# Performance work log

Measured on AMD Instinct MI355X. Metric: run time of the kernel, lower is better.

Reference implementation:

```python
import jax, jax.numpy as jnp
import numpy as np

B, N, D = 64, 1024, 1024

def setup_inputs() -> dict:
    key = jax.random.key(0)
    k1, k2, k3, k4, k5 = jax.random.split(key, 5)
    s = 1.0 / np.sqrt(D)
    return {
        "h_t": jax.random.normal(k1, (B, D), dtype=jnp.float32),
        "keys": jax.random.normal(k2, (B, N, D), dtype=jnp.float32),
        "W_h": jax.random.uniform(k3, (D, D), jnp.float32, -s, s),
        "W_k": jax.random.uniform(k4, (D, D), jnp.float32, -s, s),
        "v": jax.random.uniform(k5, (D,), jnp.float32, -s, s),
    }

def reference(h_t, keys, W_h, W_k, v):
    # W_h(h_t): [B, D]; W_k(keys): [B, N, D]  (nn.Linear computes x @ W.T)
    qh = h_t @ W_h.T                       # [B, D]
    kh = jnp.einsum('bnd,ed->bne', keys, W_k)  # [B, N, D]
    energy = jnp.tanh(qh[:, None, :] + kh)     # [B, N, D]
    scores = jnp.einsum('bnd,d->bn', energy, v)  # [B, N]
    alpha = jax.nn.softmax(scores, axis=-1)      # [B, N]
    context = jnp.einsum('bn,bnd->bd', alpha, keys)  # [B, D]
    return (context, alpha)
```

## Files before the change

kernel.cpp:

```cpp
#include <hip/hip_runtime.h>
#include <math.h>

#define BB 64
#define NN 1024
#define DD 1024

typedef __bf16 bf16x8 __attribute__((ext_vector_type(8)));
typedef _Float16 f16x8 __attribute__((ext_vector_type(8)));
typedef float f32x4 __attribute__((ext_vector_type(4)));
typedef unsigned short u16x8 __attribute__((ext_vector_type(8)));

#define GLOAD_LDS16(g, l)                                                  \
    __builtin_amdgcn_global_load_lds(                                      \
        (const __attribute__((address_space(1))) unsigned int*)(g),        \
        (__attribute__((address_space(3))) unsigned int*)(l), 16, 0, 0)

__device__ __forceinline__ float fast_tanh(float x) {
    return 1.f - 2.f / (__expf(2.f * x) + 1.f);
}


__global__ __launch_bounds__(256) void k_wk(const float* __restrict__ W_k,
                                            _Float16* __restrict__ wkT) {
    const int et = blockIdx.x;
    const int ks = blockIdx.y;
    const int t = threadIdx.x;
    const float* src = W_k + (size_t)et * 128 * DD;
    _Float16* dst = wkT + (size_t)et * 32 * 4096;
    const int p0 = t * 8;
    const int n0 = p0 >> 5;
    const int k0 = p0 & 31;
    const int ksw = (k0 >> 3) ^ ((n0 >> 1) & 3);
    for (int kt = ks * 8; kt < ks * 8 + 8; ++kt) {
#pragma unroll
        for (int r = 0; r < 2; ++r) {
            const int n = n0 + r * 64;
            const float4* s4 = (const float4*)(src + (size_t)n * DD + kt * 32 + k0);
            float4 a = s4[0], b4 = s4[1];
            f16x8 h = {(_Float16)a.x,  (_Float16)a.y,  (_Float16)a.z,  (_Float16)a.w,
                       (_Float16)b4.x, (_Float16)b4.y, (_Float16)b4.z, (_Float16)b4.w};
            *(f16x8*)(dst + (size_t)kt * 4096 + n * 32 + ksw * 8) = h;
        }
    }
}

__global__ __launch_bounds__(256) void k_qh(const float* __restrict__ h_t,
                                            const float* __restrict__ W_h,
                                            float* __restrict__ qh,
                                            float* __restrict__ scores) {
    __shared__ float hs[DD];
    __shared__ float red2[128];
    const int b = blockIdx.x;
    const int et = blockIdx.y;
    const int t = threadIdx.x;
    if (t < 128) scores[b * NN + et * 128 + t] = 0.f;
    ((float4*)hs)[t] = ((const float4*)(h_t + (size_t)b * DD))[t];
    __syncthreads();
    const int el = t & 127;
    const int half = t >> 7;
    const int e = et * 128 + el;
    const float4* wrow = (const float4*)(W_h + (size_t)e * DD) + half * 128;
    const float* hp = hs + half * 512;
    float acc = 0.f;
#pragma unroll 4
    for (int k4 = 0; k4 < 128; ++k4) {
        float4 wv = wrow[k4];
        acc = fmaf(wv.x, hp[4 * k4 + 0], acc);
        acc = fmaf(wv.y, hp[4 * k4 + 1], acc);
        acc = fmaf(wv.z, hp[4 * k4 + 2], acc);
        acc = fmaf(wv.w, hp[4 * k4 + 3], acc);
    }
    if (half == 1) red2[el] = acc;
    __syncthreads();
    if (half == 0) qh[(size_t)b * DD + e] = acc + red2[el];
}

#define SPAD2 40
__global__ __launch_bounds__(256, 3) void k_scf(const float* __restrict__ keys,
                                                const _Float16* __restrict__ wkT,
                                                const float* __restrict__ v,
                                                const float* __restrict__ qh,
                                                float* __restrict__ scores) {
    __shared__ _Float16 As[128 * SPAD2];
    __shared__ _Float16 Bs[2 * 4096];
    __shared__ float vs[128];
    __shared__ float qs[128];
    __shared__ float red[128][2];

    const int tid = threadIdx.x;
    const int cp = blockIdx.x >> 3;
    const int nt = blockIdx.x & 7;
    const int b = blockIdx.y;
    const int e0 = cp * 128;

    if (tid < 128) {
        vs[tid] = v[e0 + tid];
        qs[tid] = qh[b * DD + e0 + tid];
    }

    const float* Ag = keys + ((size_t)b * NN + nt * 128) * DD;
    const char* Bg = (const char*)(wkT + (size_t)cp * 32 * 4096) + tid * 16;
    char* BsB = (char*)Bs;

    const int w = tid >> 6, lane = tid & 63;
    const int wm = w & 1, we = w >> 1;
    const int lcol = lane & 15, quad = lane >> 4;
    const int qx8 = (quad ^ ((lcol >> 1) & 3)) * 8;
    const int srow = tid >> 1, sseg = tid & 1;
    const float* Ap = Ag + (size_t)srow * DD + sseg * 16;

    f32x4 acc[4][4];
#pragma unroll
    for (int mi = 0; mi < 4; ++mi)
#pragma unroll
        for (int ni = 0; ni < 4; ++ni) acc[mi][ni] = (f32x4){0.f, 0.f, 0.f, 0.f};

    float4 pa[4];
#pragma unroll
    for (int i = 0; i < 4; ++i) pa[i] = ((const float4*)Ap)[i];
    GLOAD_LDS16(Bg, BsB + tid * 16);
    GLOAD_LDS16(Bg + 4096, BsB + 4096 + tid * 16);

#pragma unroll 1
    for (int kt = 0; kt < 32; ++kt) {
        const int slot = kt & 1;
        __builtin_amdgcn_s_barrier();
        __builtin_amdgcn_sched_barrier(0);
        f16x8 h0 = {(_Float16)pa[0].x, (_Float16)pa[0].y, (_Float16)pa[0].z, (_Float16)pa[0].w,
                    (_Float16)pa[1].x, (_Float16)pa[1].y, (_Float16)pa[1].z, (_Float16)pa[1].w};
        f16x8 h1 = {(_Float16)pa[2].x, (_Float16)pa[2].y, (_Float16)pa[2].z, (_Float16)pa[2].w,
                    (_Float16)pa[3].x, (_Float16)pa[3].y, (_Float16)pa[3].z, (_Float16)pa[3].w};
        *(f16x8*)&As[srow * SPAD2 + sseg * 16] = h0;
        *(f16x8*)&As[srow * SPAD2 + sseg * 16 + 8] = h1;
        if (kt + 1 < 32) {
            const float* Apn = Ap + (kt + 1) * 32;
#pragma unroll
            for (int i = 0; i < 4; ++i) pa[i] = ((const float4*)Apn)[i];
            GLOAD_LDS16(Bg + (size_t)(kt + 1) * 8192, BsB + (slot ^ 1) * 8192 + tid * 16);
            GLOAD_LDS16(Bg + (size_t)(kt + 1) * 8192 + 4096,
                        BsB + (slot ^ 1) * 8192 + 4096 + tid * 16);
            asm volatile("s_waitcnt vmcnt(6) lgkmcnt(0)" ::: "memory");
        } else {
            asm volatile("s_waitcnt vmcnt(0) lgkmcnt(0)" ::: "memory");
        }
        __builtin_amdgcn_s_barrier();
        __builtin_amdgcn_sched_barrier(0);

        f16x8 af[4], bf[4];
#pragma unroll
        for (int mi = 0; mi < 4; ++mi)
            af[mi] = *(const f16x8*)&As[(wm * 64 + mi * 16 + lcol) * SPAD2 + quad * 8];
#pragma unroll
        for (int ni = 0; ni < 4; ++ni)
            bf[ni] = *(const f16x8*)&Bs[slot * 4096 + (we * 64 + ni * 16 + lcol) * 32 + qx8];
        asm volatile("s_waitcnt lgkmcnt(0)" ::: "memory");
        __builtin_amdgcn_sched_barrier(0);
        __builtin_amdgcn_s_setprio(1);
#pragma unroll
        for (int mi = 0; mi < 4; ++mi)
#pragma unroll
            for (int ni = 0; ni < 4; ++ni)
                acc[mi][ni] = __builtin_amdgcn_mfma_f32_16x16x32_f16(af[mi], bf[ni], acc[mi][ni], 0, 0, 0);
        __builtin_amdgcn_s_setprio(0);
        __builtin_amdgcn_sched_barrier(0);
    }

    float part[4][4];
#pragma unroll
    for (int mi = 0; mi < 4; ++mi)
#pragma unroll
        for (int r = 0; r < 4; ++r) part[mi][r] = 0.f;
#pragma unroll
    for (int mi = 0; mi < 4; ++mi)
#pragma unroll
        for (int ni = 0; ni < 4; ++ni) {
            const int e = we * 64 + ni * 16 + lcol;
            const float vv = vs[e];
            const float qv = qs[e];
#pragma unroll
            for (int r = 0; r < 4; ++r)
                part[mi][r] += vv * fast_tanh(qv + acc[mi][ni][r]);
        }
#pragma unroll
    for (int mi = 0; mi < 4; ++mi)
#pragma unroll
        for (int r = 0; r < 4; ++r) {
            float p = part[mi][r];
            p += __shfl_xor(p, 1);
            p += __shfl_xor(p, 2);
            p += __shfl_xor(p, 4);
            p += __shfl_xor(p, 8);
            if (lcol == 0) red[wm * 64 + mi * 16 + quad * 4 + r][we] = p;
        }
    __syncthreads();
    if (tid < 128) atomicAdd(&scores[b * NN + nt * 128 + tid], red[tid][0] + red[tid][1]);
}

__global__ __launch_bounds__(256) void k_sm(const float* __restrict__ scores,
                                            float* __restrict__ alpha) {
    const int b = blockIdx.x;
    const int t = threadIdx.x;
    float x[4];
    float m = -1e30f;
#pragma unroll
    for (int j = 0; j < 4; ++j) {
        x[j] = scores[b * NN + t + 256 * j];
        m = fmaxf(m, x[j]);
    }
#pragma unroll
    for (int mask = 32; mask >= 1; mask >>= 1) m = fmaxf(m, __shfl_xor(m, mask));
    __shared__ float wred[4];
    __shared__ float wsum[4];
    const int wv = t >> 6;
    if ((t & 63) == 0) wred[wv] = m;
    __syncthreads();
    m = fmaxf(fmaxf(wred[0], wred[1]), fmaxf(wred[2], wred[3]));
    float s = 0.f;
#pragma unroll
    for (int j = 0; j < 4; ++j) {
        x[j] = expf(x[j] - m);
        s += x[j];
    }
#pragma unroll
    for (int mask = 32; mask >= 1; mask >>= 1) s += __shfl_xor(s, mask);
    if ((t & 63) == 0) wsum[wv] = s;
    __syncthreads();
    s = wsum[0] + wsum[1] + wsum[2] + wsum[3];
    const float inv = 1.f / s;
#pragma unroll
    for (int j = 0; j < 4; ++j) alpha[b * NN + t + 256 * j] = x[j] * inv;
}

__global__ __launch_bounds__(256) void k_ctx(const float* __restrict__ keys,
                                             const float* __restrict__ alpha,
                                             float* __restrict__ context) {
    __shared__ float al[NN];
    __shared__ float red[16][72];
    const int dc = blockIdx.x;
    const int b = blockIdx.y;
    const int t = threadIdx.x;
#pragma unroll
    for (int j = 0; j < 4; ++j) al[t + 256 * j] = alpha[b * NN + t + 256 * j];
    __syncthreads();

    const int ng = t >> 4;
    const int dq = t & 15;
    const float* kp = keys + (size_t)b * NN * DD + dc * 64 + dq * 4;
    float4 acc = {0.f, 0.f, 0.f, 0.f};
#pragma unroll 4
    for (int i = 0; i < 64; ++i) {
        const int n = i * 16 + ng;
        float4 kv = *(const float4*)(kp + (size_t)n * DD);
        const float a = al[n];
        acc.x = fmaf(a, kv.x, acc.x);
        acc.y = fmaf(a, kv.y, acc.y);
        acc.z = fmaf(a, kv.z, acc.z);
        acc.w = fmaf(a, kv.w, acc.w);
    }
    *(float4*)&red[ng][dq * 4] = acc;
    __syncthreads();
    if (t < 64) {
        float s = 0.f;
#pragma unroll
        for (int g = 0; g < 16; ++g) s += red[g][t];
        context[(size_t)b * DD + dc * 64 + t] = s;
    }
}

__global__ __launch_bounds__(256) void qh_fb(const float* __restrict__ h_t,
                                             const float* __restrict__ W_h,
                                             float* __restrict__ qh,
                                             float* __restrict__ scores) {
    __shared__ float hs[DD];
    const int b = blockIdx.y;
    const int e = blockIdx.x * 256 + threadIdx.x;
    scores[(blockIdx.y * 4 + blockIdx.x) * 256 + threadIdx.x] = 0.f;
    for (int i = threadIdx.x; i < DD; i += 256) hs[i] = h_t[b * DD + i];
    __syncthreads();
    const float4* wrow = (const float4*)(W_h + (size_t)e * DD);
    float acc = 0.f;
#pragma unroll 4
    for (int k4 = 0; k4 < DD / 4; ++k4) {
        float4 w = wrow[k4];
        acc = fmaf(w.x, hs[4 * k4 + 0], acc);
        acc = fmaf(w.y, hs[4 * k4 + 1], acc);
        acc = fmaf(w.z, hs[4 * k4 + 2], acc);
        acc = fmaf(w.w, hs[4 * k4 + 3], acc);
    }
    qh[b * DD + e] = acc;
}

#define SPAD 40
__device__ __forceinline__ void split16(const float4* __restrict__ src,
                                        unsigned short* hi, unsigned short* lo) {
    float x[16];
    float4 v0 = src[0], v1 = src[1], v2 = src[2], v3 = src[3];
    x[0] = v0.x; x[1] = v0.y; x[2] = v0.z; x[3] = v0.w;
    x[4] = v1.x; x[5] = v1.y; x[6] = v1.z; x[7] = v1.w;
    x[8] = v2.x; x[9] = v2.y; x[10] = v2.z; x[11] = v2.w;
    x[12] = v3.x; x[13] = v3.y; x[14] = v3.z; x[15] = v3.w;
#pragma unroll
    for (int i = 0; i < 16; ++i) {
        unsigned int u = __float_as_uint(x[i]);
        hi[i] = (unsigned short)(u >> 16);
        float hif = __uint_as_float(u & 0xFFFF0000u);
        float lof = x[i] - hif;
        lo[i] = (unsigned short)(__float_as_uint(lof) >> 16);
    }
}

__global__ __launch_bounds__(256, 2) void scores_fb(const float* __restrict__ keys,
                                                    const float* __restrict__ W_k,
                                                    const float* __restrict__ v,
                                                    const float* __restrict__ qh,
                                                    float* __restrict__ scores) {
    __shared__ unsigned short Ah[128 * SPAD];
    __shared__ unsigned short Al[128 * SPAD];
    __shared__ unsigned short Bh[128 * SPAD];
    __shared__ unsigned short Bl[128 * SPAD];
    __shared__ float vs[128];
    __shared__ float qs[128];
    __shared__ float red[128][2];

    const int tid = threadIdx.x;
    const int cp = blockIdx.x;
    const int rt = blockIdx.y;
    const int b = rt >> 3;
    const int n0 = (rt & 7) * 128;
    const int e0 = cp * 128;
    if (tid < 128) {
        vs[tid] = v[e0 + tid];
        qs[tid] = qh[b * DD + e0 + tid];
    }
    const float* Ag = keys + ((size_t)b * NN + n0) * DD;
    const float* Bg = W_k + (size_t)e0 * DD;
    const int w = tid >> 6;
    const int lane = tid & 63;
    const int wm = w & 1;
    const int we = w >> 1;
    const int lcol = lane & 15;
    const int quad = lane >> 4;
    f32x4 acc[4][4];
#pragma unroll
    for (int mi = 0; mi < 4; ++mi)
#pragma unroll
        for (int ni = 0; ni < 4; ++ni) acc[mi][ni] = (f32x4){0.f, 0.f, 0.f, 0.f};
    const int srow = tid >> 1;
    const int sseg = tid & 1;
    float4 pa[4], pb[4];
    {
        const float4* as = (const float4*)(Ag + (size_t)srow * DD + sseg * 16);
        const float4* bs = (const float4*)(Bg + (size_t)srow * DD + sseg * 16);
#pragma unroll
        for (int i = 0; i < 4; ++i) { pa[i] = as[i]; pb[i] = bs[i]; }
    }
    for (int kt = 0; kt < DD / 32; ++kt) {
        __syncthreads();
        {
            unsigned short hi[16], lo[16];
            split16(pa, hi, lo);
            u16x8* dh = (u16x8*)&Ah[srow * SPAD + sseg * 16];
            u16x8* dl = (u16x8*)&Al[srow * SPAD + sseg * 16];
            dh[0] = *(u16x8*)&hi[0]; dh[1] = *(u16x8*)&hi[8];
            dl[0] = *(u16x8*)&lo[0]; dl[1] = *(u16x8*)&lo[8];
            split16(pb, hi, lo);
            u16x8* eh = (u16x8*)&Bh[srow * SPAD + sseg * 16];
            u16x8* el = (u16x8*)&Bl[srow * SPAD + sseg * 16];
            eh[0] = *(u16x8*)&hi[0]; eh[1] = *(u16x8*)&hi[8];
            el[0] = *(u16x8*)&lo[0]; el[1] = *(u16x8*)&lo[8];
        }
        if (kt + 1 < DD / 32) {
            const int k0 = (kt + 1) * 32;
            const float4* as = (const float4*)(Ag + (size_t)srow * DD + k0 + sseg * 16);
            const float4* bs = (const float4*)(Bg + (size_t)srow * DD + k0 + sseg * 16);
#pragma unroll
            for (int i = 0; i < 4; ++i) { pa[i] = as[i]; pb[i] = bs[i]; }
        }
        __syncthreads();
        bf16x8 ah[4], al2[4], bh[4], bl2[4];
#pragma unroll
        for (int mi = 0; mi < 4; ++mi) {
            const int r = wm * 64 + mi * 16 + lcol;
            ah[mi] = *(const bf16x8*)&Ah[r * SPAD + quad * 8];
            al2[mi] = *(const bf16x8*)&Al[r * SPAD + quad * 8];
        }
#pragma unroll
        for (int ni = 0; ni < 4; ++ni) {
            const int r = we * 64 + ni * 16 + lcol;
            bh[ni] = *(const bf16x8*)&Bh[r * SPAD + quad * 8];
            bl2[ni] = *(const bf16x8*)&Bl[r * SPAD + quad * 8];
        }
#pragma unroll
        for (int mi = 0; mi < 4; ++mi)
#pragma unroll
            for (int ni = 0; ni < 4; ++ni) {
                acc[mi][ni] = __builtin_amdgcn_mfma_f32_16x16x32_bf16(ah[mi], bh[ni], acc[mi][ni], 0, 0, 0);
                acc[mi][ni] = __builtin_amdgcn_mfma_f32_16x16x32_bf16(ah[mi], bl2[ni], acc[mi][ni], 0, 0, 0);
                acc[mi][ni] = __builtin_amdgcn_mfma_f32_16x16x32_bf16(al2[mi], bh[ni], acc[mi][ni], 0, 0, 0);
            }
    }
    float part[4][4];
#pragma unroll
    for (int mi = 0; mi < 4; ++mi)
#pragma unroll
        for (int r = 0; r < 4; ++r) part[mi][r] = 0.f;
#pragma unroll
    for (int mi = 0; mi < 4; ++mi)
#pragma unroll
        for (int ni = 0; ni < 4; ++ni) {
            const int e = we * 64 + ni * 16 + lcol;
            const float vv = vs[e];
            const float qv = qs[e];
#pragma unroll
            for (int r = 0; r < 4; ++r)
                part[mi][r] += vv * fast_tanh(qv + acc[mi][ni][r]);
        }
#pragma unroll
    for (int mi = 0; mi < 4; ++mi)
#pragma unroll
        for (int r = 0; r < 4; ++r) {
            float p = part[mi][r];
            p += __shfl_xor(p, 1);
            p += __shfl_xor(p, 2);
            p += __shfl_xor(p, 4);
            p += __shfl_xor(p, 8);
            if (lcol == 0) red[wm * 64 + mi * 16 + quad * 4 + r][we] = p;
        }
    __syncthreads();
    if (tid < 128) atomicAdd(&scores[b * NN + n0 + tid], red[tid][0] + red[tid][1]);
}

__global__ __launch_bounds__(256) void sm_fb(const float* __restrict__ scores,
                                             float* __restrict__ alpha,
                                             float* __restrict__ context) {
    const int b = blockIdx.x;
    const int t = threadIdx.x;
#pragma unroll
    for (int j = 0; j < 4; ++j) context[b * DD + t + 256 * j] = 0.f;
    float x[4];
    float m = -1e30f;
#pragma unroll
    for (int j = 0; j < 4; ++j) {
        x[j] = scores[b * NN + t + 256 * j];
        m = fmaxf(m, x[j]);
    }
#pragma unroll
    for (int mask = 32; mask >= 1; mask >>= 1) m = fmaxf(m, __shfl_xor(m, mask));
    __shared__ float wred[4];
    __shared__ float wsum[4];
    const int wv = t >> 6;
    if ((t & 63) == 0) wred[wv] = m;
    __syncthreads();
    m = fmaxf(fmaxf(wred[0], wred[1]), fmaxf(wred[2], wred[3]));
    float s = 0.f;
#pragma unroll
    for (int j = 0; j < 4; ++j) {
        x[j] = expf(x[j] - m);
        s += x[j];
    }
#pragma unroll
    for (int mask = 32; mask >= 1; mask >>= 1) s += __shfl_xor(s, mask);
    if ((t & 63) == 0) wsum[wv] = s;
    __syncthreads();
    s = wsum[0] + wsum[1] + wsum[2] + wsum[3];
    const float inv = 1.f / s;
#pragma unroll
    for (int j = 0; j < 4; ++j) alpha[b * NN + t + 256 * j] = x[j] * inv;
}

__global__ __launch_bounds__(256) void ctx_fb(const float* __restrict__ keys,
                                              const float* __restrict__ alpha,
                                              float* __restrict__ context) {
    const int b = blockIdx.y;
    const int nc = blockIdx.x;
    const int t = threadIdx.x;
    __shared__ float al[64];
    if (t < 64) al[t] = alpha[b * NN + nc * 64 + t];
    __syncthreads();
    const float4* kp = (const float4*)(keys + ((size_t)b * NN + nc * 64) * DD);
    float4 acc = {0.f, 0.f, 0.f, 0.f};
#pragma unroll 4
    for (int n = 0; n < 64; ++n) {
        const float a = al[n];
        float4 kv = kp[(size_t)n * (DD / 4) + t];
        acc.x = fmaf(a, kv.x, acc.x);
        acc.y = fmaf(a, kv.y, acc.y);
        acc.z = fmaf(a, kv.z, acc.z);
        acc.w = fmaf(a, kv.w, acc.w);
    }
    float* cp = context + b * DD + 4 * t;
    atomicAdd(cp + 0, acc.x);
    atomicAdd(cp + 1, acc.y);
    atomicAdd(cp + 2, acc.z);
    atomicAdd(cp + 3, acc.w);
}

extern "C" void kernel_launch(void* const* d_in, const int* in_sizes, int n_in,
                              void* d_out, int out_size, void* d_ws, size_t ws_size,
                              hipStream_t stream) {
    const float* h_t = (const float*)d_in[0];
    const float* keys = (const float*)d_in[1];
    const float* W_h = (const float*)d_in[2];
    const float* W_k = (const float*)d_in[3];
    const float* v = (const float*)d_in[4];

    float* context = (float*)d_out;
    float* alpha = (float*)d_out + BB * DD;
    float* qh = (float*)d_ws;
    float* scores = (float*)d_ws + BB * DD;

    const size_t wkT_off = (size_t)2 * BB * DD * sizeof(float);
    const size_t need = wkT_off + (size_t)DD * DD * 2;

    if (ws_size >= need) {
        _Float16* wkT = (_Float16*)((char*)d_ws + wkT_off);
        k_wk<<<dim3(8, 4), 256, 0, stream>>>(W_k, wkT);
        k_qh<<<dim3(64, 8), 256, 0, stream>>>(h_t, W_h, qh, scores);
        k_scf<<<dim3(64, 64), 256, 0, stream>>>(keys, wkT, v, qh, scores);
        k_sm<<<BB, 256, 0, stream>>>(scores, alpha);
        k_ctx<<<dim3(16, 64), 256, 0, stream>>>(keys, alpha, context);
    } else {
        qh_fb<<<dim3(4, BB), 256, 0, stream>>>(h_t, W_h, qh, scores);
        scores_fb<<<dim3(8, 512), 256, 0, stream>>>(keys, W_k, v, qh, scores);
        sm_fb<<<BB, 256, 0, stream>>>(scores, alpha, context);
        ctx_fb<<<dim3(16, BB), 256, 0, stream>>>(keys, alpha, context);
    }
}
```

Before: 605.8 us.

## Double K-step per iteration in score GEMM and fuse softmax into context kernel

```diff
diff --git a/kernel.cpp b/kernel.cpp
--- a/kernel.cpp
+++ b/kernel.cpp
@@ -75,14 +75,13 @@
     if (half == 0) qh[(size_t)b * DD + e] = acc + red2[el];
 }
 
-#define SPAD2 40
 __global__ __launch_bounds__(256, 3) void k_scf(const float* __restrict__ keys,
                                                 const _Float16* __restrict__ wkT,
                                                 const float* __restrict__ v,
                                                 const float* __restrict__ qh,
                                                 float* __restrict__ scores) {
-    __shared__ _Float16 As[128 * SPAD2];
-    __shared__ _Float16 Bs[2 * 4096];
+    __shared__ _Float16 As[2 * 4096];
+    __shared__ _Float16 Bs[2 * 8192];
     __shared__ float vs[128];
     __shared__ float qs[128];
     __shared__ float red[128][2];
@@ -107,7 +106,9 @@
     const int lcol = lane & 15, quad = lane >> 4;
     const int qx8 = (quad ^ ((lcol >> 1) & 3)) * 8;
     const int srow = tid >> 1, sseg = tid & 1;
-    const float* Ap = Ag + (size_t)srow * DD + sseg * 16;
+    const float* Ap = Ag + (size_t)srow * DD + sseg * 32;
+    const int awofs = sseg * 4096 + srow * 32;
+    const int aswz = (srow >> 1) & 3;
 
     f32x4 acc[4][4];
 #pragma unroll
@@ -115,54 +116,70 @@
 #pragma unroll
         for (int ni = 0; ni < 4; ++ni) acc[mi][ni] = (f32x4){0.f, 0.f, 0.f, 0.f};
 
-    float4 pa[4];
-#pragma unroll
-    for (int i = 0; i < 4; ++i) pa[i] = ((const float4*)Ap)[i];
-    GLOAD_LDS16(Bg, BsB + tid * 16);
-    GLOAD_LDS16(Bg + 4096, BsB + 4096 + tid * 16);
+    asm volatile("s_waitcnt vmcnt(0) lgkmcnt(0)" ::: "memory");
+    __builtin_amdgcn_sched_barrier(0);
+
+    float4 pa[8];
+#pragma unroll
+    for (int i = 0; i < 8; ++i) pa[i] = ((const float4*)Ap)[i];
+#pragma unroll
+    for (int r = 0; r < 4; ++r) GLOAD_LDS16(Bg + r * 4096, BsB + r * 4096 + tid * 16);
 
 #pragma unroll 1
-    for (int kt = 0; kt < 32; ++kt) {
+    for (int kt = 0; kt < 16; ++kt) {
         const int slot = kt & 1;
         __builtin_amdgcn_s_barrier();
         __builtin_amdgcn_sched_barrier(0);
-        f16x8 h0 = {(_Float16)pa[0].x, (_Float16)pa[0].y, (_Float16)pa[0].z, (_Float16)pa[0].w,
-                    (_Float16)pa[1].x, (_Float16)pa[1].y, (_Float16)pa[1].z, (_Float16)pa[1].w};
-        f16x8 h1 = {(_Float16)pa[2].x, (_Float16)pa[2].y, (_Float16)pa[2].z, (_Float16)pa[2].w,
-                    (_Float16)pa[3].x, (_Float16)pa[3].y, (_Float16)pa[3].z, (_Float16)pa[3].w};
-        *(f16x8*)&As[srow * SPAD2 + sseg * 16] = h0;
-        *(f16x8*)&As[srow * SPAD2 + sseg * 16 + 8] = h1;
-        if (kt + 1 < 32) {
-            const float* Apn = Ap + (kt + 1) * 32;
-#pragma unroll
-            for (int i = 0; i < 4; ++i) pa[i] = ((const float4*)Apn)[i];
-            GLOAD_LDS16(Bg + (size_t)(kt + 1) * 8192, BsB + (slot ^ 1) * 8192 + tid * 16);
-            GLOAD_LDS16(Bg + (size_t)(kt + 1) * 8192 + 4096,
-                        BsB + (slot ^ 1) * 8192 + 4096 + tid * 16);
-            asm volatile("s_waitcnt vmcnt(6) lgkmcnt(0)" ::: "memory");
+        {
+            f16x8 h0 = {(_Float16)pa[0].x, (_Float16)pa[0].y, (_Float16)pa[0].z, (_Float16)pa[0].w,
+                        (_Float16)pa[1].x, (_Float16)pa[1].y, (_Float16)pa[1].z, (_Float16)pa[1].w};
+            f16x8 h1 = {(_Float16)pa[2].x, (_Float16)pa[2].y, (_Float16)pa[2].z, (_Float16)pa[2].w,
+                        (_Float16)pa[3].x, (_Float16)pa[3].y, (_Float16)pa[3].z, (_Float16)pa[3].w};
+            f16x8 h2 = {(_Float16)pa[4].x, (_Float16)pa[4].y, (_Float16)pa[4].z, (_Float16)pa[4].w,
+                        (_Float16)pa[5].x, (_Float16)pa[5].y, (_Float16)pa[5].z, (_Float16)pa[5].w};
+            f16x8 h3 = {(_Float16)pa[6].x, (_Float16)pa[6].y, (_Float16)pa[6].z, (_Float16)pa[6].w,
+                        (_Float16)pa[7].x, (_Float16)pa[7].y, (_Float16)pa[7].z, (_Float16)pa[7].w};
+            *(f16x8*)&As[awofs + ((0 ^ aswz) * 8)] = h0;
+            *(f16x8*)&As[awofs + ((1 ^ aswz) * 8)] = h1;
+            *(f16x8*)&As[awofs + ((2 ^ aswz) * 8)] = h2;
+            *(f16x8*)&As[awofs + ((3 ^ aswz) * 8)] = h3;
+        }
+        if (kt + 1 < 16) {
+            const float* Apn = Ap + (size_t)(kt + 1) * 64;
+#pragma unroll
+            for (int i = 0; i < 8; ++i) pa[i] = ((const float4*)Apn)[i];
+#pragma unroll
+            for (int r = 0; r < 4; ++r)
+                GLOAD_LDS16(Bg + (size_t)(kt + 1) * 16384 + r * 4096,
+                            BsB + (slot ^ 1) * 16384 + r * 4096 + tid * 16);
+            asm volatile("s_waitcnt vmcnt(12) lgkmcnt(0)" ::: "memory");
         } else {
             asm volatile("s_waitcnt vmcnt(0) lgkmcnt(0)" ::: "memory");
         }
         __builtin_amdgcn_s_barrier();
         __builtin_amdgcn_sched_barrier(0);
 
-        f16x8 af[4], bf[4];
-#pragma unroll
-        for (int mi = 0; mi < 4; ++mi)
-            af[mi] = *(const f16x8*)&As[(wm * 64 + mi * 16 + lcol) * SPAD2 + quad * 8];
-#pragma unroll
-        for (int ni = 0; ni < 4; ++ni)
-            bf[ni] = *(const f16x8*)&Bs[slot * 4096 + (we * 64 + ni * 16 + lcol) * 32 + qx8];
-        asm volatile("s_waitcnt lgkmcnt(0)" ::: "memory");
-        __builtin_amdgcn_sched_barrier(0);
-        __builtin_amdgcn_s_setprio(1);
-#pragma unroll
-        for (int mi = 0; mi < 4; ++mi)
+#pragma unroll
+        for (int kh = 0; kh < 2; ++kh) {
+            f16x8 af[4], bf[4];
+#pragma unroll
+            for (int mi = 0; mi < 4; ++mi)
+                af[mi] = *(const f16x8*)&As[kh * 4096 + (wm * 64 + mi * 16 + lcol) * 32 + qx8];
 #pragma unroll
             for (int ni = 0; ni < 4; ++ni)
-                acc[mi][ni] = __builtin_amdgcn_mfma_f32_16x16x32_f16(af[mi], bf[ni], acc[mi][ni], 0, 0, 0);
-        __builtin_amdgcn_s_setprio(0);
-        __builtin_amdgcn_sched_barrier(0);
+                bf[ni] = *(const f16x8*)&Bs[slot * 8192 + kh * 4096 +
+                                            (we * 64 + ni * 16 + lcol) * 32 + qx8];
+            asm volatile("s_waitcnt lgkmcnt(0)" ::: "memory");
+            __builtin_amdgcn_sched_barrier(0);
+            __builtin_amdgcn_s_setprio(1);
+#pragma unroll
+            for (int mi = 0; mi < 4; ++mi)
+#pragma unroll
+                for (int ni = 0; ni < 4; ++ni)
+                    acc[mi][ni] = __builtin_amdgcn_mfma_f32_16x16x32_f16(af[mi], bf[ni], acc[mi][ni], 0, 0, 0);
+            __builtin_amdgcn_s_setprio(0);
+            __builtin_amdgcn_sched_barrier(0);
+        }
     }
 
     float part[4][4];
@@ -196,10 +213,18 @@
     if (tid < 128) atomicAdd(&scores[b * NN + nt * 128 + tid], red[tid][0] + red[tid][1]);
 }
 
-__global__ __launch_bounds__(256) void k_sm(const float* __restrict__ scores,
-                                            float* __restrict__ alpha) {
-    const int b = blockIdx.x;
+__global__ __launch_bounds__(256) void k_smctx(const float* __restrict__ scores,
+                                               const float* __restrict__ keys,
+                                               float* __restrict__ alpha,
+                                               float* __restrict__ context) {
+    __shared__ float al[NN];
+    __shared__ float red[16][72];
+    __shared__ float wred[4];
+    __shared__ float wsum[4];
+    const int dc = blockIdx.x;
+    const int b = blockIdx.y;
     const int t = threadIdx.x;
+
     float x[4];
     float m = -1e30f;
 #pragma unroll
@@ -209,8 +234,6 @@
     }
 #pragma unroll
     for (int mask = 32; mask >= 1; mask >>= 1) m = fmaxf(m, __shfl_xor(m, mask));
-    __shared__ float wred[4];
-    __shared__ float wsum[4];
     const int wv = t >> 6;
     if ((t & 63) == 0) wred[wv] = m;
     __syncthreads();
@@ -228,19 +251,11 @@
     s = wsum[0] + wsum[1] + wsum[2] + wsum[3];
     const float inv = 1.f / s;
 #pragma unroll
-    for (int j = 0; j < 4; ++j) alpha[b * NN + t + 256 * j] = x[j] * inv;
-}
-
-__global__ __launch_bounds__(256) void k_ctx(const float* __restrict__ keys,
-                                             const float* __restrict__ alpha,
-                                             float* __restrict__ context) {
-    __shared__ float al[NN];
-    __shared__ float red[16][72];
-    const int dc = blockIdx.x;
-    const int b = blockIdx.y;
-    const int t = threadIdx.x;
-#pragma unroll
-    for (int j = 0; j < 4; ++j) al[t + 256 * j] = alpha[b * NN + t + 256 * j];
+    for (int j = 0; j < 4; ++j) {
+        const float a = x[j] * inv;
+        al[t + 256 * j] = a;
+        if (dc == 0) alpha[b * NN + t + 256 * j] = a;
+    }
     __syncthreads();
 
     const int ng = t >> 4;
@@ -260,10 +275,10 @@
     *(float4*)&red[ng][dq * 4] = acc;
     __syncthreads();
     if (t < 64) {
-        float s = 0.f;
-#pragma unroll
-        for (int g = 0; g < 16; ++g) s += red[g][t];
-        context[(size_t)b * DD + dc * 64 + t] = s;
+        float sum = 0.f;
+#pragma unroll
+        for (int g = 0; g < 16; ++g) sum += red[g][t];
+        context[(size_t)b * DD + dc * 64 + t] = sum;
     }
 }
 
@@ -517,8 +532,7 @@
         k_wk<<<dim3(8, 4), 256, 0, stream>>>(W_k, wkT);
         k_qh<<<dim3(64, 8), 256, 0, stream>>>(h_t, W_h, qh, scores);
         k_scf<<<dim3(64, 64), 256, 0, stream>>>(keys, wkT, v, qh, scores);
-        k_sm<<<BB, 256, 0, stream>>>(scores, alpha);
-        k_ctx<<<dim3(16, 64), 256, 0, stream>>>(keys, alpha, context);
+        k_smctx<<<dim3(16, 64), 256, 0, stream>>>(scores, keys, alpha, context);
     } else {
         qh_fb<<<dim3(4, BB), 256, 0, stream>>>(h_t, W_h, qh, scores);
         scores_fb<<<dim3(8, 512), 256, 0, stream>>>(keys, W_k, v, qh, scores);
```

New measurement: 693.6 us. 14.5% more time.
